# Kernel tuning notes

Hardware: AMD Instinct MI355X
Metric: run time of the kernel (lower is better)

## Reference

```python
import jax, jax.numpy as jnp
import numpy as np

D, NH, NL, NP, DFF = 256, 8, 4, 4, 1024
HD = D // NH
SHAPES = np.array([[100, 152], [50, 76], [25, 38], [13, 19]], dtype=np.int64)
LV = int((SHAPES[:, 0] * SHAPES[:, 1]).sum())  # 20197


def setup_inputs() -> dict:
    key = jax.random.key(0)
    ks = iter(jax.random.split(key, 48))
    bs, Lq = 8, 300

    def w(shape, s=0.02):
        return jax.random.normal(next(ks), shape, jnp.float32) * s

    lsi = np.concatenate([[0], np.cumsum(SHAPES[:, 0] * SHAPES[:, 1])[:-1]]).astype(np.int64)
    return dict(
        tgt=w((bs, Lq, D), 1.0),
        query_pos=w((bs, Lq, D), 1.0),
        reference_points=jax.random.uniform(next(ks), (bs, Lq, NL, 2), jnp.float32),
        src=w((bs, LV, D), 1.0),
        in_proj_w=w((3 * D, D)), in_proj_b=jnp.zeros((3 * D,), jnp.float32),
        out_proj_w=w((D, D)), out_proj_b=jnp.zeros((D,), jnp.float32),
        samp_off_w=w((NH * NL * NP * 2, D)), samp_off_b=w((NH * NL * NP * 2,), 0.5),
        attn_w_w=w((NH * NL * NP, D)), attn_w_b=jnp.zeros((NH * NL * NP,), jnp.float32),
        value_proj_w=w((D, D)), value_proj_b=jnp.zeros((D,), jnp.float32),
        output_proj_w=w((D, D)), output_proj_b=jnp.zeros((D,), jnp.float32),
        lin1_w=w((DFF, D)), lin1_b=jnp.zeros((DFF,), jnp.float32),
        lin2_w=w((D, DFF)), lin2_b=jnp.zeros((D,), jnp.float32),
        norm1_w=jnp.ones((D,), jnp.float32), norm1_b=jnp.zeros((D,), jnp.float32),
        norm2_w=jnp.ones((D,), jnp.float32), norm2_b=jnp.zeros((D,), jnp.float32),
        norm3_w=jnp.ones((D,), jnp.float32), norm3_b=jnp.zeros((D,), jnp.float32),
        spatial_shapes=SHAPES,            # static numpy (shapes must be static)
        level_start_index=lsi,            # static numpy
        padding_mask=jnp.zeros((bs, LV), bool),
    )


def _ln(x, w, b):
    m = x.mean(-1, keepdims=True)
    v = ((x - m) ** 2).mean(-1, keepdims=True)
    return (x - m) * jax.lax.rsqrt(v + 1e-5) * w + b


def _bilinear(vflat, H_, W_, loc):
    # vflat: (b,h,H*W,d); loc: (b,h,q,p,2) normalized to [0,1]
    # matches F.grid_sample(align_corners=False, padding_mode='zeros')
    x = loc[..., 0] * W_ - 0.5
    y = loc[..., 1] * H_ - 0.5
    x0f, y0f = jnp.floor(x), jnp.floor(y)
    lx, ly = x - x0f, y - y0f
    x0, y0 = x0f.astype(jnp.int32), y0f.astype(jnp.int32)
    b, h, q, p = x0.shape

    def gather(ix, iy, wgt):
        valid = (ix >= 0) & (ix < W_) & (iy >= 0) & (iy < H_)
        idx = (jnp.clip(iy, 0, H_ - 1) * W_ + jnp.clip(ix, 0, W_ - 1)).reshape(b, h, q * p)
        g = jnp.take_along_axis(vflat, idx[..., None], axis=2)  # (b,h,q*p,d)
        return g * (wgt * valid).reshape(b, h, q * p, 1)

    out = (gather(x0, y0, (1 - lx) * (1 - ly)) + gather(x0 + 1, y0, lx * (1 - ly))
           + gather(x0, y0 + 1, (1 - lx) * ly) + gather(x0 + 1, y0 + 1, lx * ly))
    return out.reshape(b, h, q, p, -1)


def reference(tgt, query_pos, reference_points, src, in_proj_w, in_proj_b,
              out_proj_w, out_proj_b, samp_off_w, samp_off_b, attn_w_w, attn_w_b,
              value_proj_w, value_proj_b, output_proj_w, output_proj_b,
              lin1_w, lin1_b, lin2_w, lin2_b, norm1_w, norm1_b, norm2_w, norm2_b,
              norm3_w, norm3_b, spatial_shapes, level_start_index, padding_mask):
    bs, Lq, _ = tgt.shape
    ss = np.asarray(spatial_shapes)
    lsi = np.asarray(level_start_index)

    # ---- self attention (eval mode, dropout off) ----
    qk = tgt + query_pos
    qh = (qk @ in_proj_w[:D].T + in_proj_b[:D]).reshape(bs, Lq, NH, HD)
    kh = (qk @ in_proj_w[D:2 * D].T + in_proj_b[D:2 * D]).reshape(bs, Lq, NH, HD)
    vh = (tgt @ in_proj_w[2 * D:].T + in_proj_b[2 * D:]).reshape(bs, Lq, NH, HD)
    scores = jnp.einsum('bqhd,bkhd->bhqk', qh, kh) / jnp.sqrt(jnp.float32(HD))
    attn = jax.nn.softmax(scores, axis=-1)
    sa = jnp.einsum('bhqk,bkhd->bqhd', attn, vh).reshape(bs, Lq, D)
    sa = sa @ out_proj_w.T + out_proj_b
    x = _ln(tgt + sa, norm2_w, norm2_b)

    # ---- MSDeformAttn cross attention ----
    query = x + query_pos
    value = src @ value_proj_w.T + value_proj_b
    value = jnp.where(padding_mask[..., None], 0.0, value)
    value_t = value.reshape(bs, -1, NH, HD).transpose(0, 2, 1, 3)  # (b,h,Lv,d)

    offsets = (query @ samp_off_w.T + samp_off_b).reshape(bs, Lq, NH, NL, NP, 2)
    aw = jax.nn.softmax((query @ attn_w_w.T + attn_w_b).reshape(bs, Lq, NH, NL * NP), -1)
    aw = aw.reshape(bs, Lq, NH, NL, NP)
    norma = jnp.asarray(np.stack([ss[:, 1], ss[:, 0]], -1), jnp.float32)  # (NL,2)=[W,H]
    loc = reference_points[:, :, None, :, None, :] + offsets / norma[None, None, None, :, None, :]

    out = jnp.zeros((bs, Lq, NH, HD), value.dtype)
    for l in range(NL):
        H_, W_ = int(ss[l, 0]), int(ss[l, 1])
        s0 = int(lsi[l])
        vl = value_t[:, :, s0:s0 + H_ * W_]                    # (b,h,HW,d)
        ll = loc[:, :, :, l].transpose(0, 2, 1, 3, 4)          # (b,h,q,p,2)
        samp = _bilinear(vl, H_, W_, ll)                       # (b,h,q,p,d)
        out = out + jnp.einsum('bhqpd,bqhp->bqhd', samp, aw[:, :, :, l])
    ca = out.reshape(bs, Lq, D) @ output_proj_w.T + output_proj_b
    x = _ln(x + ca, norm1_w, norm1_b)

    # ---- FFN ----
    ffn = jax.nn.relu(x @ lin1_w.T + lin1_b) @ lin2_w.T + lin2_b
    x = _ln(x + ffn, norm3_w, norm3_b)
    return (x, loc, aw)
```

## Files before the change

kernel.cpp:

```cpp
#include <hip/hip_runtime.h>
#include <hip/hip_bf16.h>

#define D_ 256
#define NH_ 8
#define HD_ 32
#define NL_ 4
#define NP_ 4
#define DFF_ 1024
#define BS_ 8
#define LQ_ 300
#define LV_ 20197
#define NQ_ (BS_*LQ_)
#define NSRC_ (BS_*LV_*D_)

__device__ __forceinline__ float u2f(unsigned int u) {
    union { unsigned int i; float f; } v; v.i = u << 16; return v.f;
}
__device__ __forceinline__ float lo2f(unsigned int u) {
    union { unsigned int i; float f; } v; v.i = u << 16; return v.f;
}
__device__ __forceinline__ float hi2f(unsigned int u) {
    union { unsigned int i; float f; } v; v.i = u & 0xffff0000u; return v.f;
}
__device__ __forceinline__ unsigned short f2bf_bits(float f) {
    __hip_bfloat16 b = __float2bfloat16(f);
    union { __hip_bfloat16 b; unsigned short u; } v; v.b = b; return v.u;
}

#define DOT4(accum, wv, ap) do { \
    float4 _a = *(const float4*)(ap); \
    accum += wv.x*_a.x + wv.y*_a.y + wv.z*_a.z + wv.w*_a.w; } while(0)

__global__ __launch_bounds__(256) void cvt_bf16_kernel(
    const float* __restrict__ src, const float* __restrict__ wv,
    unsigned short* __restrict__ vbf, unsigned short* __restrict__ wbf)
{
    const int nsrc4 = NSRC_/4;
    const int total4 = nsrc4 + (D_*D_)/4;
    for (int i = blockIdx.x*256 + threadIdx.x; i < total4; i += gridDim.x*256) {
        float4 v;
        if (i < nsrc4) v = ((const float4*)src)[i];
        else           v = ((const float4*)wv)[i - nsrc4];
        ushort4 o;
        o.x = f2bf_bits(v.x); o.y = f2bf_bits(v.y);
        o.z = f2bf_bits(v.z); o.w = f2bf_bits(v.w);
        if (i < nsrc4) ((ushort4*)vbf)[i] = o;
        else           ((ushort4*)wbf)[i - nsrc4] = o;
    }
}

__global__ __launch_bounds__(256) void qkv_kernel(
    const float* __restrict__ tgt, const float* __restrict__ qp,
    const float* __restrict__ w, const float* __restrict__ bias,
    float* __restrict__ qh, float* __restrict__ kh, float* __restrict__ vh)
{
    __shared__ float arow[8][D_];
    const int t = threadIdx.x, m0 = blockIdx.x * 8, pass = blockIdx.y;
    for (int r = 0; r < 8; ++r) {
        float tv = tgt[(m0+r)*D_ + t];
        arow[r][t] = (pass == 2) ? tv : tv + qp[(m0+r)*D_ + t];
    }
    __syncthreads();
    const float4* w4 = (const float4*)(w + (pass*256 + t)*D_);
    float acc[8] = {0,0,0,0,0,0,0,0};
    for (int c = 0; c < 64; ++c) {
        float4 wv = w4[c];
#pragma unroll
        for (int r = 0; r < 8; ++r) DOT4(acc[r], wv, &arow[r][c*4]);
    }
    float bb = bias[pass*256 + t];
    float* dst = (pass == 0) ? qh : (pass == 1) ? kh : vh;
    for (int r = 0; r < 8; ++r) dst[(m0+r)*D_ + t] = acc[r] + bb;
}

__global__ __launch_bounds__(256) void attn_kernel(
    const float* __restrict__ qh, const float* __restrict__ kh,
    const float* __restrict__ vh, float* __restrict__ sa)
{
    __shared__ unsigned short khl[LQ_][HD_+2];
    __shared__ unsigned short vhl[LQ_][HD_+2];
    __shared__ float sc[4][LQ_];
    __shared__ float qbuf[4][HD_];
    const int b = blockIdx.x >> 3, h = blockIdx.x & 7, chunk = blockIdx.y;
    const int t = threadIdx.x, w = t >> 6, lane = t & 63;
    for (int i = t; i < LQ_*HD_; i += 256) {
        int kq = i >> 5, d = i & 31;
        khl[kq][d] = f2bf_bits(kh[(b*LQ_ + kq)*D_ + h*HD_ + d]);
        vhl[kq][d] = f2bf_bits(vh[(b*LQ_ + kq)*D_ + h*HD_ + d]);
    }
    __syncthreads();
    const float scale = 0.17677669529663687f;
    for (int qi = 0; qi < 15; ++qi) {
        const int q = chunk*60 + w*15 + qi;
        if (lane < HD_) qbuf[w][lane] = qh[(b*LQ_ + q)*D_ + h*HD_ + lane];
        float qv[HD_];
#pragma unroll
        for (int d2 = 0; d2 < HD_; ++d2) qv[d2] = qbuf[w][d2];
        float mx = -1e30f;
        for (int k = lane; k < LQ_; k += 64) {
            float s = 0.f;
#pragma unroll
            for (int d2 = 0; d2 < HD_; ++d2) s += qv[d2]*u2f(khl[k][d2]);
            s *= scale;
            sc[w][k] = s;
            mx = fmaxf(mx, s);
        }
#pragma unroll
        for (int off = 32; off; off >>= 1) mx = fmaxf(mx, __shfl_xor(mx, off));
        float lsum = 0.f;
        for (int k = lane; k < LQ_; k += 64) {
            float e = __expf(sc[w][k] - mx);
            sc[w][k] = e; lsum += e;
        }
#pragma unroll
        for (int off = 32; off; off >>= 1) lsum += __shfl_xor(lsum, off);
        const int d = lane & 31, half = lane >> 5;
        float acc = 0.f;
        for (int k = half*150; k < half*150 + 150; ++k) acc += sc[w][k]*u2f(vhl[k][d]);
        acc += __shfl_down(acc, 32);
        if (lane < 32) sa[(b*LQ_ + q)*D_ + h*HD_ + d] = acc / lsum;
    }
}

__global__ __launch_bounds__(256) void proj_res_ln_kernel(
    const float* __restrict__ A, const float* __restrict__ W,
    const float* __restrict__ bias, const float* __restrict__ res,
    const float* __restrict__ gw, const float* __restrict__ gb,
    float* __restrict__ out)
{
    __shared__ float arow[8][D_];
    __shared__ float2 part[4][8];
    const int t = threadIdx.x, m0 = blockIdx.x * 8;
    const int w = t >> 6, lane = t & 63;
    for (int r = 0; r < 8; ++r) arow[r][t] = A[(m0+r)*D_ + t];
    __syncthreads();
    float acc[8] = {0,0,0,0,0,0,0,0};
    const float4* w4 = (const float4*)(W + t*D_);
    for (int c = 0; c < 64; ++c) {
        float4 wv = w4[c];
#pragma unroll
        for (int r = 0; r < 8; ++r) DOT4(acc[r], wv, &arow[r][c*4]);
    }
    const float bb = bias[t], gwv = gw[t], gbv = gb[t];
    float v[8];
#pragma unroll
    for (int r = 0; r < 8; ++r) {
        v[r] = acc[r] + bb + res[(m0+r)*D_+t];
        float s = v[r], ss = v[r]*v[r];
#pragma unroll
        for (int off = 32; off; off >>= 1) {
            s += __shfl_xor(s, off); ss += __shfl_xor(ss, off);
        }
        if (lane == 0) part[w][r] = make_float2(s, ss);
    }
    __syncthreads();
#pragma unroll
    for (int r = 0; r < 8; ++r) {
        float2 p0 = part[0][r], p1 = part[1][r], p2 = part[2][r], p3 = part[3][r];
        float mean = (p0.x+p1.x+p2.x+p3.x) * (1.0f/256.0f);
        float ex2  = (p0.y+p1.y+p2.y+p3.y) * (1.0f/256.0f);
        float var  = ex2 - mean*mean;
        out[(m0+r)*D_+t] = (v[r]-mean) * rsqrtf(var + 1e-5f) * gwv + gbv;
    }
}

__global__ __launch_bounds__(256) void samp_params_kernel(
    const float* __restrict__ x1, const float* __restrict__ qp,
    const float* __restrict__ so_w, const float* __restrict__ so_b,
    const float* __restrict__ aw_w, const float* __restrict__ aw_b,
    const float* __restrict__ refp,
    float* __restrict__ loc_out, float* __restrict__ aw_out)
{
    __shared__ float qrow[8][D_];
    __shared__ float logits[8][128];
    const int t = threadIdx.x, m0 = blockIdx.x * 8;
    for (int r = 0; r < 8; ++r)
        qrow[r][t] = x1[(m0+r)*D_ + t] + qp[(m0+r)*D_ + t];
    __syncthreads();
    {
        float acc[8] = {0,0,0,0,0,0,0,0};
        const float4* w4 = (const float4*)(so_w + t*D_);
        for (int c = 0; c < 64; ++c) {
            float4 wv = w4[c];
#pragma unroll
            for (int r = 0; r < 8; ++r) DOT4(acc[r], wv, &qrow[r][c*4]);
        }
        const float ob = so_b[t];
        const int c_ = t & 1, l_ = (t >> 3) & 3;
        float nrm;
        if (c_ == 0) nrm = (l_==0)?152.f:(l_==1)?76.f:(l_==2)?38.f:19.f;
        else         nrm = (l_==0)?100.f:(l_==1)?50.f:(l_==2)?25.f:13.f;
        for (int r = 0; r < 8; ++r) {
            int m = m0 + r;
            float off = acc[r] + ob;
            loc_out[m*256 + t] = refp[(m*NL_ + l_)*2 + c_] + off / nrm;
        }
    }
    if (t < 128) {
        float acc[8] = {0,0,0,0,0,0,0,0};
        const float4* w4 = (const float4*)(aw_w + t*D_);
        for (int c = 0; c < 64; ++c) {
            float4 wv = w4[c];
#pragma unroll
            for (int r = 0; r < 8; ++r) DOT4(acc[r], wv, &qrow[r][c*4]);
        }
        const float ab = aw_b[t];
        for (int r = 0; r < 8; ++r) logits[r][t] = acc[r] + ab;
    }
    __syncthreads();
    if (t < 128) {
        const int g0 = (t >> 4) << 4;
        for (int r = 0; r < 8; ++r) {
            float mx = -1e30f;
            for (int j = 0; j < 16; ++j) mx = fmaxf(mx, logits[r][g0+j]);
            float s = 0.f;
            for (int j = 0; j < 16; ++j) s += __expf(logits[r][g0+j] - mx);
            aw_out[(m0+r)*128 + t] = __expf(logits[r][t] - mx) / s;
        }
    }
}

__global__ __launch_bounds__(256) void samp_fuse_bf16_kernel(
    const unsigned short* __restrict__ vbf,
    const float* __restrict__ loc_f, const float* __restrict__ aw_f,
    float* __restrict__ svec_g, float* __restrict__ wsum_g)
{
    __shared__ int   cidx[128][4];
    __shared__ float cwt[128][4];
    const int m = blockIdx.x, t = threadIdx.x;
    const int b = m / LQ_;

    if (t < 128) {
        const int l = (t >> 2) & 3;
        const int HS[4] = {100,50,25,13}, WS[4] = {152,76,38,19}, S0[4] = {0,15200,19000,19950};
        const int Hh = HS[l], Ww = WS[l], s0 = S0[l];
        const float aw = aw_f[m*128 + t];
        const float x = loc_f[m*256 + 2*t]*Ww - 0.5f;
        const float y = loc_f[m*256 + 2*t + 1]*Hh - 0.5f;
        const float x0f = floorf(x), y0f = floorf(y);
        const int x0 = (int)x0f, y0 = (int)y0f;
        const float fx = x - x0f, fy = y - y0f;
        const int   cx[4] = {x0, x0+1, x0,   x0+1};
        const int   cy[4] = {y0, y0,   y0+1, y0+1};
        const float cw[4] = {(1.f-fx)*(1.f-fy), fx*(1.f-fy), (1.f-fx)*fy, fx*fy};
        float sw = 0.f;
#pragma unroll
        for (int j = 0; j < 4; ++j) {
            const bool valid = (cx[j] >= 0) & (cx[j] < Ww) & (cy[j] >= 0) & (cy[j] < Hh);
            cidx[t][j] = valid ? (s0 + cy[j]*Ww + cx[j]) : s0;
            float wv = valid ? aw*cw[j] : 0.f;
            cwt[t][j] = wv;
            sw += wv;
        }
#pragma unroll
        for (int off = 8; off; off >>= 1) sw += __shfl_xor(sw, off);
        if ((t & 15) == 0) wsum_g[m*NH_ + (t >> 4)] = sw;
    }
    __syncthreads();

    const int hh = (t >> 7) * 4;
    const int c  = t & 127;
    const unsigned int* sb = (const unsigned int*)(vbf + (size_t)b*LV_*D_) + c;
#pragma unroll
    for (int h = hh; h < hh + 4; ++h) {
        float e0=0.f, e1=0.f, e2=0.f, e3=0.f;
        float o0=0.f, o1=0.f, o2=0.f, o3=0.f;
#pragma unroll 4
        for (int s = 0; s < 16; ++s) {
            const int base = h*16 + s;
            const int   i0 = cidx[base][0], i1 = cidx[base][1],
                        i2 = cidx[base][2], i3 = cidx[base][3];
            const float w0 = cwt[base][0], w1 = cwt[base][1],
                        w2 = cwt[base][2], w3 = cwt[base][3];
            const unsigned int u0 = sb[(size_t)i0*128];
            const unsigned int u1 = sb[(size_t)i1*128];
            const unsigned int u2 = sb[(size_t)i2*128];
            const unsigned int u3 = sb[(size_t)i3*128];
            e0 += w0*lo2f(u0); o0 += w0*hi2f(u0);
            e1 += w1*lo2f(u1); o1 += w1*hi2f(u1);
            e2 += w2*lo2f(u2); o2 += w2*hi2f(u2);
            e3 += w3*lo2f(u3); o3 += w3*hi2f(u3);
        }
        *(float2*)&svec_g[(size_t)m*(NH_*D_) + h*D_ + 2*c] =
            make_float2((e0+e1)+(e2+e3), (o0+o1)+(o2+o3));
    }
}

__global__ __launch_bounds__(256) void vproj_kernel(
    const float* __restrict__ svec_g, const float* __restrict__ wsum_g,
    const unsigned short* __restrict__ wbf, const float* __restrict__ vpb,
    float* __restrict__ vo)
{
    __shared__ float sv[4][NH_*D_];
    const int t = threadIdx.x, m0 = blockIdx.x * 4;
    for (int i = t; i < 4*NH_*D_; i += 256)
        sv[i >> 11][i & 2047] = svec_g[(size_t)m0*(NH_*D_) + i];
    __syncthreads();
    const int h = t >> 5;
    const ushort4* w4 = (const ushort4*)(wbf + t*D_);
    float a0 = 0.f, a1 = 0.f, a2 = 0.f, a3 = 0.f;
    for (int c = 0; c < 64; ++c) {
        const ushort4 wq = w4[c];
        const float wx = u2f(wq.x), wy = u2f(wq.y), wz = u2f(wq.z), ww = u2f(wq.w);
        const float4 s0 = *(const float4*)&sv[0][h*D_ + c*4];
        const float4 s1 = *(const float4*)&sv[1][h*D_ + c*4];
        const float4 s2 = *(const float4*)&sv[2][h*D_ + c*4];
        const float4 s3 = *(const float4*)&sv[3][h*D_ + c*4];
        a0 += wx*s0.x + wy*s0.y + wz*s0.z + ww*s0.w;
        a1 += wx*s1.x + wy*s1.y + wz*s1.z + ww*s1.w;
        a2 += wx*s2.x + wy*s2.y + wz*s2.z + ww*s2.w;
        a3 += wx*s3.x + wy*s3.y + wz*s3.z + ww*s3.w;
    }
    const float bb = vpb[t];
    vo[(size_t)(m0+0)*D_ + t] = a0 + bb*wsum_g[(m0+0)*NH_ + h];
    vo[(size_t)(m0+1)*D_ + t] = a1 + bb*wsum_g[(m0+1)*NH_ + h];
    vo[(size_t)(m0+2)*D_ + t] = a2 + bb*wsum_g[(m0+2)*NH_ + h];
    vo[(size_t)(m0+3)*D_ + t] = a3 + bb*wsum_g[(m0+3)*NH_ + h];
}

__global__ __launch_bounds__(256) void samp_fuse_f32_kernel(
    const float* __restrict__ src, const float* __restrict__ Wv,
    const float* __restrict__ vpb,
    const float* __restrict__ loc_f, const float* __restrict__ aw_f,
    float* __restrict__ vo)
{
    __shared__ float svec[NH_][D_];
    __shared__ int   cidx[128][4];
    __shared__ float cwt[128][4];
    __shared__ float wsum[NH_];
    const int m = blockIdx.x, t = threadIdx.x;
    const int b = m / LQ_;

    if (t < 128) {
        const int l = (t >> 2) & 3;
        const int HS[4] = {100,50,25,13}, WS[4] = {152,76,38,19}, S0[4] = {0,15200,19000,19950};
        const int Hh = HS[l], Ww = WS[l], s0 = S0[l];
        const float aw = aw_f[m*128 + t];
        const float x = loc_f[m*256 + 2*t]*Ww - 0.5f;
        const float y = loc_f[m*256 + 2*t + 1]*Hh - 0.5f;
        const float x0f = floorf(x), y0f = floorf(y);
        const int x0 = (int)x0f, y0 = (int)y0f;
        const float fx = x - x0f, fy = y - y0f;
        const int   cx[4] = {x0, x0+1, x0,   x0+1};
        const int   cy[4] = {y0, y0,   y0+1, y0+1};
        const float cw[4] = {(1.f-fx)*(1.f-fy), fx*(1.f-fy), (1.f-fx)*fy, fx*fy};
        float sw = 0.f;
#pragma unroll
        for (int jj = 0; jj < 4; ++jj) {
            const bool valid = (cx[jj] >= 0) & (cx[jj] < Ww) & (cy[jj] >= 0) & (cy[jj] < Hh);
            cidx[t][jj] = valid ? (s0 + cy[jj]*Ww + cx[jj]) : s0;
            float wv = valid ? aw*cw[jj] : 0.f;
            cwt[t][jj] = wv;
            sw += wv;
        }
#pragma unroll
        for (int off = 8; off; off >>= 1) sw += __shfl_xor(sw, off);
        if ((t & 15) == 0) wsum[t >> 4] = sw;
    }
    __syncthreads();

    const float* sb = src + (size_t)b*LV_*D_ + t;
#pragma unroll
    for (int h = 0; h < NH_; ++h) {
        float a0 = 0.f, a1 = 0.f, a2 = 0.f, a3 = 0.f;
#pragma unroll 4
        for (int s = 0; s < 16; ++s) {
            const int base = h*16 + s;
            const int   i0 = cidx[base][0], i1 = cidx[base][1],
                        i2 = cidx[base][2], i3 = cidx[base][3];
            const float w0 = cwt[base][0], w1 = cwt[base][1],
                        w2 = cwt[base][2], w3 = cwt[base][3];
            a0 += w0 * sb[(size_t)i0*D_];
            a1 += w1 * sb[(size_t)i1*D_];
            a2 += w2 * sb[(size_t)i2*D_];
            a3 += w3 * sb[(size_t)i3*D_];
        }
        svec[h][t] = (a0 + a1) + (a2 + a3);
    }
    __syncthreads();

    const int h = t >> 5;
    const float4* w4 = (const float4*)(Wv + t*D_);
    float a = 0.f;
    for (int c = 0; c < 64; ++c) {
        float4 wv = w4[c];
        DOT4(a, wv, &svec[h][c*4]);
    }
    vo[m*D_ + t] = a + vpb[t]*wsum[h];
}

__global__ __launch_bounds__(256) void ffn1_kernel(
    const float* __restrict__ x2, const float* __restrict__ W1,
    const float* __restrict__ b1, float* __restrict__ hid)
{
    __shared__ float arow[8][D_];
    const int t = threadIdx.x, m0 = blockIdx.x * 8, cc = blockIdx.y;
    for (int r = 0; r < 8; ++r) arow[r][t] = x2[(m0+r)*D_ + t];
    __syncthreads();
    const int j = cc*256 + t;
    float acc[8] = {0,0,0,0,0,0,0,0};
    const float4* w4 = (const float4*)(W1 + j*D_);
    for (int c = 0; c < 64; ++c) {
        float4 wv = w4[c];
#pragma unroll
        for (int r = 0; r < 8; ++r) DOT4(acc[r], wv, &arow[r][c*4]);
    }
    const float bb = b1[j];
    for (int r = 0; r < 8; ++r) {
        float v = acc[r] + bb;
        hid[(m0+r)*DFF_ + j] = v > 0.f ? v : 0.f;
    }
}

__global__ __launch_bounds__(256) void ffn2_ln_kernel(
    const float* __restrict__ hid, const float* __restrict__ W2,
    const float* __restrict__ b2, const float* __restrict__ res,
    const float* __restrict__ gw, const float* __restrict__ gb,
    float* __restrict__ out)
{
    __shared__ float hrow[8][DFF_];
    __shared__ float2 part[4][8];
    const int t = threadIdx.x, m0 = blockIdx.x * 8;
    const int w = t >> 6, lane = t & 63;
    for (int i = t; i < 8*DFF_; i += 256)
        hrow[i >> 10][i & 1023] = hid[(m0 + (i >> 10))*DFF_ + (i & 1023)];
    __syncthreads();
    float acc[8] = {0,0,0,0,0,0,0,0};
    const float4* w4 = (const float4*)(W2 + t*DFF_);
    for (int c = 0; c < 256; ++c) {
        float4 wv = w4[c];
#pragma unroll
        for (int r = 0; r < 8; ++r) DOT4(acc[r], wv, &hrow[r][c*4]);
    }
    const float bb = b2[t], gwv = gw[t], gbv = gb[t];
    float v[8];
#pragma unroll
    for (int r = 0; r < 8; ++r) {
        v[r] = acc[r] + bb + res[(m0+r)*D_+t];
        float s = v[r], ss = v[r]*v[r];
#pragma unroll
        for (int off = 32; off; off >>= 1) {
            s += __shfl_xor(s, off); ss += __shfl_xor(ss, off);
        }
        if (lane == 0) part[w][r] = make_float2(s, ss);
    }
    __syncthreads();
#pragma unroll
    for (int r = 0; r < 8; ++r) {
        float2 p0 = part[0][r], p1 = part[1][r], p2 = part[2][r], p3 = part[3][r];
        float mean = (p0.x+p1.x+p2.x+p3.x) * (1.0f/256.0f);
        float ex2  = (p0.y+p1.y+p2.y+p3.y) * (1.0f/256.0f);
        float var  = ex2 - mean*mean;
        out[(m0+r)*D_+t] = (v[r]-mean) * rsqrtf(var + 1e-5f) * gwv + gbv;
    }
}

extern "C" void kernel_launch(void* const* d_in, const int* in_sizes, int n_in,
                              void* d_out, int out_size, void* d_ws, size_t ws_size,
                              hipStream_t stream) {
    (void)in_sizes; (void)n_in; (void)out_size;
    const float* tgt  = (const float*)d_in[0];
    const float* qpos = (const float*)d_in[1];
    const float* refp = (const float*)d_in[2];
    const float* srcp = (const float*)d_in[3];
    const float* ipw  = (const float*)d_in[4];
    const float* ipb  = (const float*)d_in[5];
    const float* opw  = (const float*)d_in[6];
    const float* opb  = (const float*)d_in[7];
    const float* sow  = (const float*)d_in[8];
    const float* sob  = (const float*)d_in[9];
    const float* aww  = (const float*)d_in[10];
    const float* awb  = (const float*)d_in[11];
    const float* vpw  = (const float*)d_in[12];
    const float* vpb  = (const float*)d_in[13];
    const float* outw = (const float*)d_in[14];
    const float* outb = (const float*)d_in[15];
    const float* l1w  = (const float*)d_in[16];
    const float* l1b  = (const float*)d_in[17];
    const float* l2w  = (const float*)d_in[18];
    const float* l2b  = (const float*)d_in[19];
    const float* n1w  = (const float*)d_in[20];
    const float* n1b  = (const float*)d_in[21];
    const float* n2w  = (const float*)d_in[22];
    const float* n2b  = (const float*)d_in[23];
    const float* n3w  = (const float*)d_in[24];
    const float* n3b  = (const float*)d_in[25];

    float* wsf = (float*)d_ws;
    float* qh   = wsf;
    float* kh   = wsf + 614400;
    float* vh   = wsf + 1228800;
    float* sa   = wsf + 1843200;
    float* x1   = wsf + 2457600;
    float* vo   = wsf + 3072000;
    float* x2   = wsf + 3686400;
    float* hid  = wsf + 4300800;
    unsigned short* vbf = (unsigned short*)(wsf + 6758400);
    unsigned short* wbf = (unsigned short*)(wsf + 6758400 + 20681728);
    float* svec_g = wsf + 6758400 + 20681728 + 32768;
    float* wsum_g = svec_g + 4915200;
    const size_t need_bytes = (size_t)(6758400 + 20681728 + 32768 + 4915200 + 19200) * 4;
    const bool use_bf16 = ws_size >= need_bytes;

    float* xout   = (float*)d_out;
    float* locout = xout + 614400;
    float* awout  = xout + 1228800;

    if (use_bf16)
        cvt_bf16_kernel<<<2048, 256, 0, stream>>>(srcp, vpw, vbf, wbf);
    qkv_kernel<<<dim3(NQ_/8, 3), 256, 0, stream>>>(tgt, qpos, ipw, ipb, qh, kh, vh);
    attn_kernel<<<dim3(BS_*NH_, 5), 256, 0, stream>>>(qh, kh, vh, sa);
    proj_res_ln_kernel<<<NQ_/8, 256, 0, stream>>>(sa, opw, opb, tgt, n2w, n2b, x1);
    samp_params_kernel<<<NQ_/8, 256, 0, stream>>>(x1, qpos, sow, sob, aww, awb, refp,
                                                  locout, awout);
    if (use_bf16) {
        samp_fuse_bf16_kernel<<<NQ_, 256, 0, stream>>>(vbf, locout, awout, svec_g, wsum_g);
        vproj_kernel<<<NQ_/4, 256, 0, stream>>>(svec_g, wsum_g, wbf, vpb, vo);
    } else {
        samp_fuse_f32_kernel<<<NQ_, 256, 0, stream>>>(srcp, vpw, vpb, locout, awout, vo);
    }
    proj_res_ln_kernel<<<NQ_/8, 256, 0, stream>>>(vo, outw, outb, x1, n1w, n1b, x2);
    ffn1_kernel<<<dim3(NQ_/8, 4), 256, 0, stream>>>(x2, l1w, l1b, hid);
    ffn2_ln_kernel<<<NQ_/8, 256, 0, stream>>>(hid, l2w, l2b, x2, n3w, n3b, xout);
}
```

Measured before the change: 654.7 us.

## Raise parallelism across GEMM, attention and sampling kernels

The GEMM-style kernels move to 512 threads per block, with each half of the block computing 4 of the 8 rows, so each thread carries fewer accumulators and more waves are in flight. The self-attention grid grows from 5 to 15 query chunks per (batch, head). The sampling kernel splits its heads across a second grid dimension, maps blocks batch-interleaved, and switches to 64-lane uint2 gathers of 4 bf16 values each. The aim is to fill the GPU better and raise memory-level parallelism. The cost is that each weight row is now loaded by two threads per block, and the sampling offsets and weights are computed twice per query.

```diff
diff --git a/kernel.cpp b/kernel.cpp
--- a/kernel.cpp
+++ b/kernel.cpp
@@ -49,28 +49,30 @@
     }
 }
 
-__global__ __launch_bounds__(256) void qkv_kernel(
+__global__ __launch_bounds__(512) void qkv_kernel(
     const float* __restrict__ tgt, const float* __restrict__ qp,
     const float* __restrict__ w, const float* __restrict__ bias,
     float* __restrict__ qh, float* __restrict__ kh, float* __restrict__ vh)
 {
     __shared__ float arow[8][D_];
     const int t = threadIdx.x, m0 = blockIdx.x * 8, pass = blockIdx.y;
-    for (int r = 0; r < 8; ++r) {
-        float tv = tgt[(m0+r)*D_ + t];
-        arow[r][t] = (pass == 2) ? tv : tv + qp[(m0+r)*D_ + t];
-    }
-    __syncthreads();
-    const float4* w4 = (const float4*)(w + (pass*256 + t)*D_);
-    float acc[8] = {0,0,0,0,0,0,0,0};
+    const int tt = t & 255, half = t >> 8;
+    for (int i = t; i < 8*D_; i += 512) {
+        int r = i >> 8, c = i & 255;
+        float tv = tgt[(m0+r)*D_ + c];
+        arow[r][c] = (pass == 2) ? tv : tv + qp[(m0+r)*D_ + c];
+    }
+    __syncthreads();
+    const float4* w4 = (const float4*)(w + (pass*256 + tt)*D_);
+    float acc[4] = {0,0,0,0};
     for (int c = 0; c < 64; ++c) {
         float4 wv = w4[c];
 #pragma unroll
-        for (int r = 0; r < 8; ++r) DOT4(acc[r], wv, &arow[r][c*4]);
-    }
-    float bb = bias[pass*256 + t];
+        for (int r = 0; r < 4; ++r) DOT4(acc[r], wv, &arow[half*4+r][c*4]);
+    }
+    float bb = bias[pass*256 + tt];
     float* dst = (pass == 0) ? qh : (pass == 1) ? kh : vh;
-    for (int r = 0; r < 8; ++r) dst[(m0+r)*D_ + t] = acc[r] + bb;
+    for (int r = 0; r < 4; ++r) dst[(m0+half*4+r)*D_ + tt] = acc[r] + bb;
 }
 
 __global__ __launch_bounds__(256) void attn_kernel(
@@ -90,8 +92,8 @@
     }
     __syncthreads();
     const float scale = 0.17677669529663687f;
-    for (int qi = 0; qi < 15; ++qi) {
-        const int q = chunk*60 + w*15 + qi;
+    for (int qi = 0; qi < 5; ++qi) {
+        const int q = chunk*20 + w*5 + qi;
         if (lane < HD_) qbuf[w][lane] = qh[(b*LQ_ + q)*D_ + h*HD_ + lane];
         float qv[HD_];
 #pragma unroll
@@ -122,30 +124,32 @@
     }
 }
 
-__global__ __launch_bounds__(256) void proj_res_ln_kernel(
+__global__ __launch_bounds__(512) void proj_res_ln_kernel(
     const float* __restrict__ A, const float* __restrict__ W,
     const float* __restrict__ bias, const float* __restrict__ res,
     const float* __restrict__ gw, const float* __restrict__ gb,
     float* __restrict__ out)
 {
     __shared__ float arow[8][D_];
-    __shared__ float2 part[4][8];
+    __shared__ float2 part[8][4];
     const int t = threadIdx.x, m0 = blockIdx.x * 8;
+    const int tt = t & 255, half = t >> 8;
     const int w = t >> 6, lane = t & 63;
-    for (int r = 0; r < 8; ++r) arow[r][t] = A[(m0+r)*D_ + t];
-    __syncthreads();
-    float acc[8] = {0,0,0,0,0,0,0,0};
-    const float4* w4 = (const float4*)(W + t*D_);
+    for (int i = t; i < 8*D_; i += 512)
+        arow[i >> 8][i & 255] = A[(m0 + (i >> 8))*D_ + (i & 255)];
+    __syncthreads();
+    float acc[4] = {0,0,0,0};
+    const float4* w4 = (const float4*)(W + tt*D_);
     for (int c = 0; c < 64; ++c) {
         float4 wv = w4[c];
 #pragma unroll
-        for (int r = 0; r < 8; ++r) DOT4(acc[r], wv, &arow[r][c*4]);
-    }
-    const float bb = bias[t], gwv = gw[t], gbv = gb[t];
-    float v[8];
-#pragma unroll
-    for (int r = 0; r < 8; ++r) {
-        v[r] = acc[r] + bb + res[(m0+r)*D_+t];
+        for (int r = 0; r < 4; ++r) DOT4(acc[r], wv, &arow[half*4+r][c*4]);
+    }
+    const float bb = bias[tt], gwv = gw[tt], gbv = gb[tt];
+    float v[4];
+#pragma unroll
+    for (int r = 0; r < 4; ++r) {
+        v[r] = acc[r] + bb + res[(m0+half*4+r)*D_+tt];
         float s = v[r], ss = v[r]*v[r];
 #pragma unroll
         for (int off = 32; off; off >>= 1) {
@@ -155,16 +159,17 @@
     }
     __syncthreads();
 #pragma unroll
-    for (int r = 0; r < 8; ++r) {
-        float2 p0 = part[0][r], p1 = part[1][r], p2 = part[2][r], p3 = part[3][r];
+    for (int r = 0; r < 4; ++r) {
+        float2 p0 = part[half*4+0][r], p1 = part[half*4+1][r],
+               p2 = part[half*4+2][r], p3 = part[half*4+3][r];
         float mean = (p0.x+p1.x+p2.x+p3.x) * (1.0f/256.0f);
         float ex2  = (p0.y+p1.y+p2.y+p3.y) * (1.0f/256.0f);
         float var  = ex2 - mean*mean;
-        out[(m0+r)*D_+t] = (v[r]-mean) * rsqrtf(var + 1e-5f) * gwv + gbv;
-    }
-}
-
-__global__ __launch_bounds__(256) void samp_params_kernel(
+        out[(m0+half*4+r)*D_+tt] = (v[r]-mean) * rsqrtf(var + 1e-5f) * gwv + gbv;
+    }
+}
+
+__global__ __launch_bounds__(512) void samp_params_kernel(
     const float* __restrict__ x1, const float* __restrict__ qp,
     const float* __restrict__ so_w, const float* __restrict__ so_b,
     const float* __restrict__ aw_w, const float* __restrict__ aw_b,
@@ -174,48 +179,52 @@
     __shared__ float qrow[8][D_];
     __shared__ float logits[8][128];
     const int t = threadIdx.x, m0 = blockIdx.x * 8;
-    for (int r = 0; r < 8; ++r)
-        qrow[r][t] = x1[(m0+r)*D_ + t] + qp[(m0+r)*D_ + t];
+    const int tt = t & 255, half = t >> 8;
+    for (int i = t; i < 8*D_; i += 512) {
+        int r = i >> 8, c = i & 255;
+        qrow[r][c] = x1[(m0+r)*D_ + c] + qp[(m0+r)*D_ + c];
+    }
     __syncthreads();
     {
-        float acc[8] = {0,0,0,0,0,0,0,0};
-        const float4* w4 = (const float4*)(so_w + t*D_);
+        float acc[4] = {0,0,0,0};
+        const float4* w4 = (const float4*)(so_w + tt*D_);
         for (int c = 0; c < 64; ++c) {
             float4 wv = w4[c];
 #pragma unroll
-            for (int r = 0; r < 8; ++r) DOT4(acc[r], wv, &qrow[r][c*4]);
-        }
-        const float ob = so_b[t];
-        const int c_ = t & 1, l_ = (t >> 3) & 3;
+            for (int r = 0; r < 4; ++r) DOT4(acc[r], wv, &qrow[half*4+r][c*4]);
+        }
+        const float ob = so_b[tt];
+        const int c_ = tt & 1, l_ = (tt >> 3) & 3;
         float nrm;
         if (c_ == 0) nrm = (l_==0)?152.f:(l_==1)?76.f:(l_==2)?38.f:19.f;
         else         nrm = (l_==0)?100.f:(l_==1)?50.f:(l_==2)?25.f:13.f;
-        for (int r = 0; r < 8; ++r) {
-            int m = m0 + r;
+        for (int r = 0; r < 4; ++r) {
+            int m = m0 + half*4 + r;
             float off = acc[r] + ob;
-            loc_out[m*256 + t] = refp[(m*NL_ + l_)*2 + c_] + off / nrm;
-        }
-    }
-    if (t < 128) {
-        float acc[8] = {0,0,0,0,0,0,0,0};
-        const float4* w4 = (const float4*)(aw_w + t*D_);
+            loc_out[m*256 + tt] = refp[(m*NL_ + l_)*2 + c_] + off / nrm;
+        }
+    }
+    if (tt < 128) {
+        float acc[4] = {0,0,0,0};
+        const float4* w4 = (const float4*)(aw_w + tt*D_);
         for (int c = 0; c < 64; ++c) {
             float4 wv = w4[c];
 #pragma unroll
-            for (int r = 0; r < 8; ++r) DOT4(acc[r], wv, &qrow[r][c*4]);
-        }
-        const float ab = aw_b[t];
-        for (int r = 0; r < 8; ++r) logits[r][t] = acc[r] + ab;
-    }
-    __syncthreads();
-    if (t < 128) {
-        const int g0 = (t >> 4) << 4;
-        for (int r = 0; r < 8; ++r) {
+            for (int r = 0; r < 4; ++r) DOT4(acc[r], wv, &qrow[half*4+r][c*4]);
+        }
+        const float ab = aw_b[tt];
+        for (int r = 0; r < 4; ++r) logits[half*4+r][tt] = acc[r] + ab;
+    }
+    __syncthreads();
+    if (tt < 128) {
+        const int g0 = (tt >> 4) << 4;
+        for (int r = 0; r < 4; ++r) {
+            const int row = half*4 + r;
             float mx = -1e30f;
-            for (int j = 0; j < 16; ++j) mx = fmaxf(mx, logits[r][g0+j]);
+            for (int j = 0; j < 16; ++j) mx = fmaxf(mx, logits[row][g0+j]);
             float s = 0.f;
-            for (int j = 0; j < 16; ++j) s += __expf(logits[r][g0+j] - mx);
-            aw_out[(m0+r)*128 + t] = __expf(logits[r][t] - mx) / s;
+            for (int j = 0; j < 16; ++j) s += __expf(logits[row][g0+j] - mx);
+            aw_out[(m0+row)*128 + tt] = __expf(logits[row][tt] - mx) / s;
         }
     }
 }
@@ -227,8 +236,9 @@
 {
     __shared__ int   cidx[128][4];
     __shared__ float cwt[128][4];
-    const int m = blockIdx.x, t = threadIdx.x;
-    const int b = m / LQ_;
+    const int t = threadIdx.x;
+    const int m = (blockIdx.x & 7)*LQ_ + (blockIdx.x >> 3);
+    const int b = blockIdx.x & 7;
 
     if (t < 128) {
         const int l = (t >> 2) & 3;
@@ -254,36 +264,33 @@
         }
 #pragma unroll
         for (int off = 8; off; off >>= 1) sw += __shfl_xor(sw, off);
-        if ((t & 15) == 0) wsum_g[m*NH_ + (t >> 4)] = sw;
-    }
-    __syncthreads();
-
-    const int hh = (t >> 7) * 4;
-    const int c  = t & 127;
-    const unsigned int* sb = (const unsigned int*)(vbf + (size_t)b*LV_*D_) + c;
-#pragma unroll
-    for (int h = hh; h < hh + 4; ++h) {
-        float e0=0.f, e1=0.f, e2=0.f, e3=0.f;
-        float o0=0.f, o1=0.f, o2=0.f, o3=0.f;
+        if (blockIdx.y == 0 && (t & 15) == 0) wsum_g[m*NH_ + (t >> 4)] = sw;
+    }
+    __syncthreads();
+
+    const int g = t >> 6, lane = t & 63;
+    const int h = blockIdx.y*4 + g;
+    const uint2* sp = (const uint2*)(vbf + (size_t)b*LV_*D_);
+    float a0=0.f,a1=0.f,a2=0.f,a3=0.f;
+    float b0=0.f,b1=0.f,b2=0.f,b3=0.f;
 #pragma unroll 4
-        for (int s = 0; s < 16; ++s) {
-            const int base = h*16 + s;
-            const int   i0 = cidx[base][0], i1 = cidx[base][1],
-                        i2 = cidx[base][2], i3 = cidx[base][3];
-            const float w0 = cwt[base][0], w1 = cwt[base][1],
-                        w2 = cwt[base][2], w3 = cwt[base][3];
-            const unsigned int u0 = sb[(size_t)i0*128];
-            const unsigned int u1 = sb[(size_t)i1*128];
-            const unsigned int u2 = sb[(size_t)i2*128];
-            const unsigned int u3 = sb[(size_t)i3*128];
-            e0 += w0*lo2f(u0); o0 += w0*hi2f(u0);
-            e1 += w1*lo2f(u1); o1 += w1*hi2f(u1);
-            e2 += w2*lo2f(u2); o2 += w2*hi2f(u2);
-            e3 += w3*lo2f(u3); o3 += w3*hi2f(u3);
-        }
-        *(float2*)&svec_g[(size_t)m*(NH_*D_) + h*D_ + 2*c] =
-            make_float2((e0+e1)+(e2+e3), (o0+o1)+(o2+o3));
-    }
+    for (int s = 0; s < 16; ++s) {
+        const int base = h*16 + s;
+        const int   i0 = cidx[base][0], i1 = cidx[base][1],
+                    i2 = cidx[base][2], i3 = cidx[base][3];
+        const float w0 = cwt[base][0], w1 = cwt[base][1],
+                    w2 = cwt[base][2], w3 = cwt[base][3];
+        const uint2 u0 = sp[(size_t)i0*64 + lane];
+        const uint2 u1 = sp[(size_t)i1*64 + lane];
+        const uint2 u2 = sp[(size_t)i2*64 + lane];
+        const uint2 u3 = sp[(size_t)i3*64 + lane];
+        a0 += w0*lo2f(u0.x); a1 += w0*hi2f(u0.x); a2 += w0*lo2f(u0.y); a3 += w0*hi2f(u0.y);
+        b0 += w1*lo2f(u1.x); b1 += w1*hi2f(u1.x); b2 += w1*lo2f(u1.y); b3 += w1*hi2f(u1.y);
+        a0 += w2*lo2f(u2.x); a1 += w2*hi2f(u2.x); a2 += w2*lo2f(u2.y); a3 += w2*hi2f(u2.y);
+        b0 += w3*lo2f(u3.x); b1 += w3*hi2f(u3.x); b2 += w3*lo2f(u3.y); b3 += w3*hi2f(u3.y);
+    }
+    *(float4*)&svec_g[(size_t)m*(NH_*D_) + h*D_ + 4*lane] =
+        make_float4(a0+b0, a1+b1, a2+b2, a3+b3);
 }
 
 __global__ __launch_bounds__(256) void vproj_kernel(
@@ -389,54 +396,57 @@
     vo[m*D_ + t] = a + vpb[t]*wsum[h];
 }
 
-__global__ __launch_bounds__(256) void ffn1_kernel(
+__global__ __launch_bounds__(512) void ffn1_kernel(
     const float* __restrict__ x2, const float* __restrict__ W1,
     const float* __restrict__ b1, float* __restrict__ hid)
 {
     __shared__ float arow[8][D_];
     const int t = threadIdx.x, m0 = blockIdx.x * 8, cc = blockIdx.y;
-    for (int r = 0; r < 8; ++r) arow[r][t] = x2[(m0+r)*D_ + t];
-    __syncthreads();
-    const int j = cc*256 + t;
-    float acc[8] = {0,0,0,0,0,0,0,0};
+    const int tt = t & 255, half = t >> 8;
+    for (int i = t; i < 8*D_; i += 512)
+        arow[i >> 8][i & 255] = x2[(m0 + (i >> 8))*D_ + (i & 255)];
+    __syncthreads();
+    const int j = cc*256 + tt;
+    float acc[4] = {0,0,0,0};
     const float4* w4 = (const float4*)(W1 + j*D_);
     for (int c = 0; c < 64; ++c) {
         float4 wv = w4[c];
 #pragma unroll
-        for (int r = 0; r < 8; ++r) DOT4(acc[r], wv, &arow[r][c*4]);
+        for (int r = 0; r < 4; ++r) DOT4(acc[r], wv, &arow[half*4+r][c*4]);
     }
     const float bb = b1[j];
-    for (int r = 0; r < 8; ++r) {
+    for (int r = 0; r < 4; ++r) {
         float v = acc[r] + bb;
-        hid[(m0+r)*DFF_ + j] = v > 0.f ? v : 0.f;
-    }
-}
-
-__global__ __launch_bounds__(256) void ffn2_ln_kernel(
+        hid[(m0+half*4+r)*DFF_ + j] = v > 0.f ? v : 0.f;
+    }
+}
+
+__global__ __launch_bounds__(512) void ffn2_ln_kernel(
     const float* __restrict__ hid, const float* __restrict__ W2,
     const float* __restrict__ b2, const float* __restrict__ res,
     const float* __restrict__ gw, const float* __restrict__ gb,
     float* __restrict__ out)
 {
     __shared__ float hrow[8][DFF_];
-    __shared__ float2 part[4][8];
+    __shared__ float2 part[8][4];
     const int t = threadIdx.x, m0 = blockIdx.x * 8;
+    const int tt = t & 255, half = t >> 8;
     const int w = t >> 6, lane = t & 63;
-    for (int i = t; i < 8*DFF_; i += 256)
+    for (int i = t; i < 8*DFF_; i += 512)
         hrow[i >> 10][i & 1023] = hid[(m0 + (i >> 10))*DFF_ + (i & 1023)];
     __syncthreads();
-    float acc[8] = {0,0,0,0,0,0,0,0};
-    const float4* w4 = (const float4*)(W2 + t*DFF_);
+    float acc[4] = {0,0,0,0};
+    const float4* w4 = (const float4*)(W2 + tt*DFF_);
     for (int c = 0; c < 256; ++c) {
         float4 wv = w4[c];
 #pragma unroll
-        for (int r = 0; r < 8; ++r) DOT4(acc[r], wv, &hrow[r][c*4]);
-    }
-    const float bb = b2[t], gwv = gw[t], gbv = gb[t];
-    float v[8];
-#pragma unroll
-    for (int r = 0; r < 8; ++r) {
-        v[r] = acc[r] + bb + res[(m0+r)*D_+t];
+        for (int r = 0; r < 4; ++r) DOT4(acc[r], wv, &hrow[half*4+r][c*4]);
+    }
+    const float bb = b2[tt], gwv = gw[tt], gbv = gb[tt];
+    float v[4];
+#pragma unroll
+    for (int r = 0; r < 4; ++r) {
+        v[r] = acc[r] + bb + res[(m0+half*4+r)*D_+tt];
         float s = v[r], ss = v[r]*v[r];
 #pragma unroll
         for (int off = 32; off; off >>= 1) {
@@ -446,12 +456,13 @@
     }
     __syncthreads();
 #pragma unroll
-    for (int r = 0; r < 8; ++r) {
-        float2 p0 = part[0][r], p1 = part[1][r], p2 = part[2][r], p3 = part[3][r];
+    for (int r = 0; r < 4; ++r) {
+        float2 p0 = part[half*4+0][r], p1 = part[half*4+1][r],
+               p2 = part[half*4+2][r], p3 = part[half*4+3][r];
         float mean = (p0.x+p1.x+p2.x+p3.x) * (1.0f/256.0f);
         float ex2  = (p0.y+p1.y+p2.y+p3.y) * (1.0f/256.0f);
         float var  = ex2 - mean*mean;
-        out[(m0+r)*D_+t] = (v[r]-mean) * rsqrtf(var + 1e-5f) * gwv + gbv;
+        out[(m0+half*4+r)*D_+tt] = (v[r]-mean) * rsqrtf(var + 1e-5f) * gwv + gbv;
     }
 }
 
@@ -508,18 +519,19 @@
 
     if (use_bf16)
         cvt_bf16_kernel<<<2048, 256, 0, stream>>>(srcp, vpw, vbf, wbf);
-    qkv_kernel<<<dim3(NQ_/8, 3), 256, 0, stream>>>(tgt, qpos, ipw, ipb, qh, kh, vh);
-    attn_kernel<<<dim3(BS_*NH_, 5), 256, 0, stream>>>(qh, kh, vh, sa);
-    proj_res_ln_kernel<<<NQ_/8, 256, 0, stream>>>(sa, opw, opb, tgt, n2w, n2b, x1);
-    samp_params_kernel<<<NQ_/8, 256, 0, stream>>>(x1, qpos, sow, sob, aww, awb, refp,
+    qkv_kernel<<<dim3(NQ_/8, 3), 512, 0, stream>>>(tgt, qpos, ipw, ipb, qh, kh, vh);
+    attn_kernel<<<dim3(BS_*NH_, 15), 256, 0, stream>>>(qh, kh, vh, sa);
+    proj_res_ln_kernel<<<NQ_/8, 512, 0, stream>>>(sa, opw, opb, tgt, n2w, n2b, x1);
+    samp_params_kernel<<<NQ_/8, 512, 0, stream>>>(x1, qpos, sow, sob, aww, awb, refp,
                                                   locout, awout);
     if (use_bf16) {
-        samp_fuse_bf16_kernel<<<NQ_, 256, 0, stream>>>(vbf, locout, awout, svec_g, wsum_g);
+        samp_fuse_bf16_kernel<<<dim3(NQ_, 2), 256, 0, stream>>>(vbf, locout, awout,
+                                                                svec_g, wsum_g);
         vproj_kernel<<<NQ_/4, 256, 0, stream>>>(svec_g, wsum_g, wbf, vpb, vo);
     } else {
         samp_fuse_f32_kernel<<<NQ_, 256, 0, stream>>>(srcp, vpw, vpb, locout, awout, vo);
     }
-    proj_res_ln_kernel<<<NQ_/8, 256, 0, stream>>>(vo, outw, outb, x1, n1w, n1b, x2);
-    ffn1_kernel<<<dim3(NQ_/8, 4), 256, 0, stream>>>(x2, l1w, l1b, hid);
-    ffn2_ln_kernel<<<NQ_/8, 256, 0, stream>>>(hid, l2w, l2b, x2, n3w, n3b, xout);
-}
+    proj_res_ln_kernel<<<NQ_/8, 512, 0, stream>>>(vo, outw, outb, x1, n1w, n1b, x2);
+    ffn1_kernel<<<dim3(NQ_/8, 4), 512, 0, stream>>>(x2, l1w, l1b, hid);
+    ffn2_ln_kernel<<<NQ_/8, 512, 0, stream>>>(hid, l2w, l2b, x2, n3w, n3b, xout);
+}
```

After: 807.0 us. 23.3% more time.
